# Performance work log

Measured on AMD Instinct MI355X. Metric: run time of the kernel, lower is better.

## Reference

```python
import jax, jax.numpy as jnp
import numpy as np
from functools import reduce

H = W = 4096


def setup_inputs() -> dict:
    key = jax.random.key(0)
    prob = jax.random.uniform(key, (1, 1, H, W), dtype=jnp.float32)
    return {"prob": prob}


def _ccl_8conn(binary):
    """Parallel connected-component labeling, 8-connectivity (skimage connectivity=2).

    Labels are (min linear index in component) + 1; background = 0. This is the
    same partition into components as skimage.measure.label, up to a bijective
    relabeling of the positive label ids.
    Algorithm: iterate [3x3 min-propagation + 2x pointer jumping] until fixpoint
    (label-equivalence / union-find style, O(log diameter)-ish sweeps).
    """
    h, w = binary.shape
    BIG = np.int32(h * w + 2)  # sentinel larger than any valid label
    idx = jnp.arange(h * w, dtype=jnp.int32).reshape(h, w) + 1
    lab0 = jnp.where(binary, idx, 0)

    def sweep(lab):
        # min over 3x3 foreground neighborhood (includes self)
        l = jnp.where(binary, lab, BIG)
        p = jnp.pad(l, 1, constant_values=int(BIG))
        neigh = [p[di:di + h, dj:dj + w] for di in range(3) for dj in range(3)]
        m = reduce(jnp.minimum, neigh)
        m = jnp.where(binary, m, 0)
        # pointer jumping: hop to the label of the pixel we currently point at
        flat = m.reshape(-1)
        for _ in range(2):
            flat = jnp.where(flat > 0, flat[jnp.maximum(flat - 1, 0)], 0)
        return flat.reshape(h, w)

    def cond(c):
        return c[1]

    def body(c):
        lab, _ = c
        new = sweep(lab)
        return new, jnp.any(new != lab)

    lab, _ = jax.lax.while_loop(cond, body, (lab0, jnp.array(True)))
    return lab


def reference(prob):
    binary = jnp.squeeze(prob) > 0.5  # (prob > 0.5).float().squeeze()
    return _ccl_8conn(binary)
```

## Files before the change

kernel.cpp:

```cpp
#include <hip/hip_runtime.h>
#include <limits.h>


constexpr int HH = 4096;
constexpr int WW = 4096;
constexpr int NPIX = HH * WW;
constexpr int TILE = 128;
constexpr int BDIM = TILE / 2;
constexpr int NBLK = BDIM * BDIM;
constexpr int NBOUND = HH / TILE - 1;
constexpr int NSEG = WW / 2;
constexpr int LINKS_PER_FAM = NBOUND * NSEG * 3;

__device__ __forceinline__ int find_root_g(int* P, int x) {
    while (true) {
        int p = P[x];
        if (p == x) return x;
        int gp = P[p];
        if (gp == p) return p;
        atomicMin(&P[x], gp);
        x = gp;
    }
}

__device__ __forceinline__ void unite_g(int* P, int a, int b) {
    while (true) {
        a = find_root_g(P, a);
        b = find_root_g(P, b);
        if (a == b) return;
        if (a > b) { int t = a; a = b; b = t; }
        int old = atomicMin(&P[b], a);
        if (old == b) return;
        b = old;
    }
}

__device__ __forceinline__ int lkey2b(int k) {
    return ((k >> 8) << 6) | ((k & 127) >> 1);
}

__device__ __forceinline__ int find_l(int* par, int bk) {
    while (true) {
        int xb = lkey2b(bk);
        int p = par[xb];
        if (p == bk) return bk;
        int pb = lkey2b(p);
        int gp = par[pb];
        if (gp == p) return p;
        atomicMin(&par[xb], gp);
        bk = gp;
    }
}

__device__ __forceinline__ void unite_l(int* par, int ka, int kb) {
    while (true) {
        ka = find_l(par, ka);
        kb = find_l(par, kb);
        if (ka == kb) return;
        if (ka > kb) { int t = ka; ka = kb; kb = t; }
        int old = atomicMin(&par[lkey2b(kb)], ka);
        if (old == kb) return;
        kb = old;
    }
}

__device__ __forceinline__ int bkey(int b, int m) {
    int base = ((b >> 6) << 8) + ((b & 63) << 1);
    int off = (m & 1) ? 0 : (m & 2) ? 1 : (m & 4) ? 128 : 129;
    return base + off;
}

__global__ __launch_bounds__(512) void ccl_local_bke(const float* __restrict__ prob,
                                                     int* __restrict__ P) {
    __shared__ int bmask[NBLK];
    __shared__ int par[NBLK];
    const int tile_c = blockIdx.x * TILE;
    const int tile_r = blockIdx.y * TILE;
    const int tid = threadIdx.x;

    int nib[8];
    #pragma unroll
    for (int k = 0; k < 8; ++k) {
        int b = tid + 512 * k;
        int i = b >> 6, j = b & 63;
        const float* rp = prob + (size_t)(tile_r + 2 * i) * WW + tile_c + 2 * j;
        float2 t = *reinterpret_cast<const float2*>(rp);
        float2 bo = *reinterpret_cast<const float2*>(rp + WW);
        int m = (t.x > 0.5f ? 1 : 0) | (t.y > 0.5f ? 2 : 0) |
                (bo.x > 0.5f ? 4 : 0) | (bo.y > 0.5f ? 8 : 0);
        nib[k] = m;
        bmask[b] = m;
        par[b] = m ? bkey(b, m) : -1;
    }
    __syncthreads();

    #pragma unroll
    for (int k = 0; k < 8; ++k) {
        int m = nib[k];
        if (!m) continue;
        int b = tid + 512 * k;
        int i = b >> 6, j = b & 63;
        int mk = bkey(b, m);
        if (j > 0) {
            int wm = bmask[b - 1];
            if ((m & 0x5) && (wm & 0xA)) unite_l(par, mk, bkey(b - 1, wm));
        }
        if (i > 0) {
            int nm = bmask[b - BDIM];
            if ((m & 0x3) && (nm & 0xC)) unite_l(par, mk, bkey(b - BDIM, nm));
            if (j > 0) {
                int nwm = bmask[b - BDIM - 1];
                if ((m & 0x1) && (nwm & 0x8)) unite_l(par, mk, bkey(b - BDIM - 1, nwm));
            }
            if (j < BDIM - 1) {
                int nem = bmask[b - BDIM + 1];
                if ((m & 0x2) && (nem & 0x4)) unite_l(par, mk, bkey(b - BDIM + 1, nem));
            }
        }
    }
    __syncthreads();

    #pragma unroll
    for (int k = 0; k < 8; ++k) {
        int b = tid + 512 * k;
        int i = b >> 6, j = b & 63;
        int gr = tile_r + 2 * i, gc = tile_c + 2 * j;
        int m = nib[k];
        int2 top = make_int2(-1, -1), bot = make_int2(-1, -1);
        if (m) {
            int x = bkey(b, m);
            while (true) {
                int p = par[lkey2b(x)];
                if (p == x) break;
                x = p;
            }
            int g = (tile_r + (x >> 7)) * WW + tile_c + (x & 127);
            top.x = (m & 1) ? g : -1;
            top.y = (m & 2) ? g : -1;
            bot.x = (m & 4) ? g : -1;
            bot.y = (m & 8) ? g : -1;
        }
        *reinterpret_cast<int2*>(P + (size_t)gr * WW + gc) = top;
        *reinterpret_cast<int2*>(P + (size_t)(gr + 1) * WW + gc) = bot;
    }
}

__global__ void ccl_border(int* __restrict__ P) {
    int idx = blockIdx.x * 256 + threadIdx.x;
    if (idx >= LINKS_PER_FAM) return;
    int link = idx / (NBOUND * NSEG);
    int rem  = idx - link * (NBOUND * NSEG);
    int bidx = rem >> 11;
    int t    = rem & (NSEG - 1);
    if (blockIdx.y == 0) {
        int r = (bidx + 1) * TILE;
        int c0 = 2 * t;
        if (link == 0) {
            int2 d = *reinterpret_cast<const int2*>(P + (size_t)r * WW + c0);
            int2 u = *reinterpret_cast<const int2*>(P + (size_t)(r - 1) * WW + c0);
            bool d0 = d.x >= 0, d1 = d.y >= 0;
            bool u0 = u.x >= 0, u1 = u.y >= 0;
            if ((d0 | d1) && (u0 | u1)) {
                int pd = d0 ? r * WW + c0 : r * WW + c0 + 1;
                int pu = u0 ? (r - 1) * WW + c0 : (r - 1) * WW + c0 + 1;
                unite_g(P, pd, pu);
            }
        } else if (link == 1) {
            if (c0 > 0 && P[(size_t)r * WW + c0] >= 0 &&
                P[(size_t)(r - 1) * WW + c0 - 1] >= 0)
                unite_g(P, r * WW + c0, (r - 1) * WW + c0 - 1);
        } else {
            if (c0 + 2 < WW && P[(size_t)r * WW + c0 + 1] >= 0 &&
                P[(size_t)(r - 1) * WW + c0 + 2] >= 0)
                unite_g(P, r * WW + c0 + 1, (r - 1) * WW + c0 + 2);
        }
    } else {
        int c = (bidx + 1) * TILE;
        int r0 = 2 * t;
        if (link == 0) {
            bool e0 = P[(size_t)r0 * WW + c] >= 0;
            bool e1 = P[(size_t)(r0 + 1) * WW + c] >= 0;
            bool w0 = P[(size_t)r0 * WW + c - 1] >= 0;
            bool w1 = P[(size_t)(r0 + 1) * WW + c - 1] >= 0;
            if ((e0 | e1) && (w0 | w1)) {
                int pe = e0 ? r0 * WW + c : (r0 + 1) * WW + c;
                int pw = w0 ? r0 * WW + c - 1 : (r0 + 1) * WW + c - 1;
                unite_g(P, pe, pw);
            }
        } else if (link == 1) {
            if (r0 > 0 && P[(size_t)r0 * WW + c] >= 0 &&
                P[(size_t)(r0 - 1) * WW + c - 1] >= 0)
                unite_g(P, r0 * WW + c, (r0 - 1) * WW + c - 1);
        } else {
            if (r0 + 2 < HH && P[(size_t)(r0 + 1) * WW + c] >= 0 &&
                P[(size_t)(r0 + 2) * WW + c - 1] >= 0)
                unite_g(P, (r0 + 1) * WW + c, (r0 + 2) * WW + c - 1);
        }
    }
}

__device__ __forceinline__ int resolve_memo(const int* __restrict__ P, int x,
                                            int& ci, int& co) {
    if (x < 0) return 0;
    if (x == ci) return co;
    int r = x;
    while (true) { int p = P[r]; if (p == r) break; r = p; }
    ci = x; co = r + 1;
    return co;
}

__global__ void ccl_final4(const int* __restrict__ P, int* __restrict__ out) {
    int i = (blockIdx.x * blockDim.x + threadIdx.x) * 4;
    int4 v = *reinterpret_cast<const int4*>(P + i);
    int ci = -2, co = 0;
    int4 o;
    o.x = resolve_memo(P, v.x, ci, co);
    o.y = resolve_memo(P, v.y, ci, co);
    o.z = resolve_memo(P, v.z, ci, co);
    o.w = resolve_memo(P, v.w, ci, co);
    *reinterpret_cast<int4*>(out + i) = o;
}

__global__ void ccl_compress(int* __restrict__ P) {
    int i = blockIdx.x * blockDim.x + threadIdx.x;
    int x = P[i];
    if (x < 0) return;
    while (true) { int p = P[x]; if (p == x) break; x = p; }
    P[i] = x;
}

__global__ void ccl_convert(int* __restrict__ P) {
    int i = (blockIdx.x * blockDim.x + threadIdx.x) * 4;
    int4 v = *reinterpret_cast<const int4*>(P + i);
    v.x = (v.x < 0) ? 0 : v.x + 1;
    v.y = (v.y < 0) ? 0 : v.y + 1;
    v.z = (v.z < 0) ? 0 : v.z + 1;
    v.w = (v.w < 0) ? 0 : v.w + 1;
    *reinterpret_cast<int4*>(P + i) = v;
}

extern "C" void kernel_launch(void* const* d_in, const int* in_sizes, int n_in,
                              void* d_out, int out_size, void* d_ws, size_t ws_size,
                              hipStream_t stream) {
    const float* prob = (const float*)d_in[0];
    const bool have_ws = ws_size >= (size_t)NPIX * sizeof(int);
    int* P = have_ws ? (int*)d_ws : (int*)d_out;

    ccl_local_bke<<<dim3(WW / TILE, HH / TILE), dim3(512), 0, stream>>>(prob, P);

    ccl_border<<<dim3((LINKS_PER_FAM + 255) / 256, 2), dim3(256), 0, stream>>>(P);

    if (have_ws) {
        ccl_final4<<<dim3(NPIX / 4 / 256), dim3(256), 0, stream>>>(P, (int*)d_out);
    } else {
        ccl_compress<<<dim3(NPIX / 256), dim3(256), 0, stream>>>(P);
        ccl_convert<<<dim3(NPIX / 4 / 256), dim3(256), 0, stream>>>(P);
    }
}
```

Measured before the change: 287.4 us.

## Merge border link families per thread and prune redundant unions

The border-merge kernel now handles 4 consecutive boundary pixels per thread instead of one 2-pixel segment per link family. Each thread loads the neighbour labels once with vector loads and reads the stored root labels directly. It skips unions that are already implied by 8-connectivity of adjacent foreground pixels, except at tile-corner positions. This cuts thread count, redundant loads and atomic union traffic, at the cost of more per-thread branching and some uncoalesced strided loads on the vertical boundaries.

Measured after the change: 241.1 us. 1.19x faster.

```diff
diff --git a/kernel.cpp b/kernel.cpp
--- a/kernel.cpp
+++ b/kernel.cpp
@@ -9,8 +9,9 @@
 constexpr int BDIM = TILE / 2;
 constexpr int NBLK = BDIM * BDIM;
 constexpr int NBOUND = HH / TILE - 1;
-constexpr int NSEG = WW / 2;
-constexpr int LINKS_PER_FAM = NBOUND * NSEG * 3;
+constexpr int SEGW = 4;
+constexpr int NSEG4 = WW / SEGW;
+constexpr int THREADS_PER_FAM = NBOUND * NSEG4;
 
 __device__ __forceinline__ int find_root_g(int* P, int x) {
     while (true) {
@@ -147,54 +148,60 @@
 
 __global__ void ccl_border(int* __restrict__ P) {
     int idx = blockIdx.x * 256 + threadIdx.x;
-    if (idx >= LINKS_PER_FAM) return;
-    int link = idx / (NBOUND * NSEG);
-    int rem  = idx - link * (NBOUND * NSEG);
-    int bidx = rem >> 11;
-    int t    = rem & (NSEG - 1);
+    if (idx >= THREADS_PER_FAM) return;
+    int bidx = idx >> 10;
+    int t    = idx & (NSEG4 - 1);
+    int dpar[6], upar[6];
     if (blockIdx.y == 0) {
         int r = (bidx + 1) * TILE;
-        int c0 = 2 * t;
-        if (link == 0) {
-            int2 d = *reinterpret_cast<const int2*>(P + (size_t)r * WW + c0);
-            int2 u = *reinterpret_cast<const int2*>(P + (size_t)(r - 1) * WW + c0);
-            bool d0 = d.x >= 0, d1 = d.y >= 0;
-            bool u0 = u.x >= 0, u1 = u.y >= 0;
-            if ((d0 | d1) && (u0 | u1)) {
-                int pd = d0 ? r * WW + c0 : r * WW + c0 + 1;
-                int pu = u0 ? (r - 1) * WW + c0 : (r - 1) * WW + c0 + 1;
-                unite_g(P, pd, pu);
-            }
-        } else if (link == 1) {
-            if (c0 > 0 && P[(size_t)r * WW + c0] >= 0 &&
-                P[(size_t)(r - 1) * WW + c0 - 1] >= 0)
-                unite_g(P, r * WW + c0, (r - 1) * WW + c0 - 1);
-        } else {
-            if (c0 + 2 < WW && P[(size_t)r * WW + c0 + 1] >= 0 &&
-                P[(size_t)(r - 1) * WW + c0 + 2] >= 0)
-                unite_g(P, r * WW + c0 + 1, (r - 1) * WW + c0 + 2);
+        int c0 = SEGW * t;
+        const int* pd = P + (size_t)r * WW;
+        const int* pu = pd - WW;
+        int4 dv = *reinterpret_cast<const int4*>(pd + c0);
+        int4 uv = *reinterpret_cast<const int4*>(pu + c0);
+        dpar[0] = (c0 > 0) ? pd[c0 - 1] : -1;
+        upar[0] = (c0 > 0) ? pu[c0 - 1] : -1;
+        dpar[1] = dv.x; dpar[2] = dv.y; dpar[3] = dv.z; dpar[4] = dv.w;
+        upar[1] = uv.x; upar[2] = uv.y; upar[3] = uv.z; upar[4] = uv.w;
+        dpar[5] = (c0 + SEGW < WW) ? pd[c0 + SEGW] : -1;
+        upar[5] = (c0 + SEGW < WW) ? pu[c0 + SEGW] : -1;
+        #pragma unroll
+        for (int k = 1; k <= SEGW; ++k) {
+            if (dpar[k] < 0) continue;
+            int c = c0 + k - 1;
+            int j = c & (TILE - 1);
+            bool U  = upar[k] >= 0;
+            bool Dm = dpar[k - 1] >= 0, Um = upar[k - 1] >= 0;
+            bool Dp = dpar[k + 1] >= 0, Up = upar[k + 1] >= 0;
+            if (U  && (j == 0        || !(Dm && Um))) unite_g(P, dpar[k], upar[k]);
+            if (Um && (j == 0        || (!U && !Dm))) unite_g(P, dpar[k], upar[k - 1]);
+            if (Up && (j == TILE - 1 || (!U && !Dp))) unite_g(P, dpar[k], upar[k + 1]);
         }
     } else {
         int c = (bidx + 1) * TILE;
-        int r0 = 2 * t;
-        if (link == 0) {
-            bool e0 = P[(size_t)r0 * WW + c] >= 0;
-            bool e1 = P[(size_t)(r0 + 1) * WW + c] >= 0;
-            bool w0 = P[(size_t)r0 * WW + c - 1] >= 0;
-            bool w1 = P[(size_t)(r0 + 1) * WW + c - 1] >= 0;
-            if ((e0 | e1) && (w0 | w1)) {
-                int pe = e0 ? r0 * WW + c : (r0 + 1) * WW + c;
-                int pw = w0 ? r0 * WW + c - 1 : (r0 + 1) * WW + c - 1;
-                unite_g(P, pe, pw);
-            }
-        } else if (link == 1) {
-            if (r0 > 0 && P[(size_t)r0 * WW + c] >= 0 &&
-                P[(size_t)(r0 - 1) * WW + c - 1] >= 0)
-                unite_g(P, r0 * WW + c, (r0 - 1) * WW + c - 1);
-        } else {
-            if (r0 + 2 < HH && P[(size_t)(r0 + 1) * WW + c] >= 0 &&
-                P[(size_t)(r0 + 2) * WW + c - 1] >= 0)
-                unite_g(P, (r0 + 1) * WW + c, (r0 + 2) * WW + c - 1);
+        int r0 = SEGW * t;
+        const int* pe = P + c;
+        const int* pw = P + c - 1;
+        dpar[0] = (r0 > 0) ? pe[(size_t)(r0 - 1) * WW] : -1;
+        upar[0] = (r0 > 0) ? pw[(size_t)(r0 - 1) * WW] : -1;
+        #pragma unroll
+        for (int k = 1; k <= SEGW; ++k) {
+            dpar[k] = pe[(size_t)(r0 + k - 1) * WW];
+            upar[k] = pw[(size_t)(r0 + k - 1) * WW];
+        }
+        dpar[5] = (r0 + SEGW < HH) ? pe[(size_t)(r0 + SEGW) * WW] : -1;
+        upar[5] = (r0 + SEGW < HH) ? pw[(size_t)(r0 + SEGW) * WW] : -1;
+        #pragma unroll
+        for (int k = 1; k <= SEGW; ++k) {
+            if (dpar[k] < 0) continue;
+            int r = r0 + k - 1;
+            int i = r & (TILE - 1);
+            bool W  = upar[k] >= 0;
+            bool Em = dpar[k - 1] >= 0, Wm = upar[k - 1] >= 0;
+            bool Ep = dpar[k + 1] >= 0, Wp = upar[k + 1] >= 0;
+            if (W  && (i == 0        || !(Em && Wm))) unite_g(P, dpar[k], upar[k]);
+            if (Wm && (i == 0        || (!W && !Em))) unite_g(P, dpar[k], upar[k - 1]);
+            if (Wp && (i == TILE - 1 || (!W && !Ep))) unite_g(P, dpar[k], upar[k + 1]);
         }
     }
 }
@@ -248,7 +255,7 @@
 
     ccl_local_bke<<<dim3(WW / TILE, HH / TILE), dim3(512), 0, stream>>>(prob, P);
 
-    ccl_border<<<dim3((LINKS_PER_FAM + 255) / 256, 2), dim3(256), 0, stream>>>(P);
+    ccl_border<<<dim3((THREADS_PER_FAM + 255) / 256, 2), dim3(256), 0, stream>>>(P);
 
     if (have_ws) {
         ccl_final4<<<dim3(NPIX / 4 / 256), dim3(256), 0, stream>>>(P, (int*)d_out);
```

## Store labels per 2x2 block with packed nibble masks for border and final passes

Applied to the files above, without the earlier changes.

The global union-find array is shrunk to one entry per 2x2 block, indexed by a key-to-block mapping, and each block's foreground nibble is packed eight to a 32-bit word. The border merge now loads the bitmasks, builds 32-bit edge masks and only unites at run starts, so each boundary segment needs far fewer thread slots and memory reads. The final pass resolves eight pixels per thread from the block-level parent array and the nibble bits. This cuts intermediate memory traffic roughly fourfold, at the cost of bit-manipulation complexity. A pixel-level fallback path is kept for when workspace is too small.

New measurement: 296.0 us. +3.0%, slower.

```diff
diff --git a/kernel.cpp b/kernel.cpp
--- a/kernel.cpp
+++ b/kernel.cpp
@@ -8,28 +8,34 @@
 constexpr int TILE = 128;
 constexpr int BDIM = TILE / 2;
 constexpr int NBLK = BDIM * BDIM;
+constexpr int BW = WW / 2;
+constexpr int WPR = BW / 8;
 constexpr int NBOUND = HH / TILE - 1;
-constexpr int NSEG = WW / 2;
-constexpr int LINKS_PER_FAM = NBOUND * NSEG * 3;
-
-__device__ __forceinline__ int find_root_g(int* P, int x) {
-    while (true) {
-        int p = P[x];
-        if (p == x) return x;
-        int gp = P[p];
+constexpr int BTHREADS = NBOUND * (WW / 32);
+
+__device__ __forceinline__ int blkof(int key) {
+    return ((key >> 13) << 11) | ((key & 4095) >> 1);
+}
+
+__device__ __forceinline__ int find_B(int* P, int key) {
+    while (true) {
+        int xb = blkof(key);
+        int p = P[xb];
+        if (p == key) return key;
+        int gp = P[blkof(p)];
         if (gp == p) return p;
-        atomicMin(&P[x], gp);
-        x = gp;
-    }
-}
-
-__device__ __forceinline__ void unite_g(int* P, int a, int b) {
-    while (true) {
-        a = find_root_g(P, a);
-        b = find_root_g(P, b);
+        atomicMin(&P[xb], gp);
+        key = gp;
+    }
+}
+
+__device__ __forceinline__ void unite_B(int* P, int a, int b) {
+    while (true) {
+        a = find_B(P, a);
+        b = find_B(P, b);
         if (a == b) return;
         if (a > b) { int t = a; a = b; b = t; }
-        int old = atomicMin(&P[b], a);
+        int old = atomicMin(&P[blkof(b)], a);
         if (old == b) return;
         b = old;
     }
@@ -71,11 +77,14 @@
 }
 
 __global__ __launch_bounds__(512) void ccl_local_bke(const float* __restrict__ prob,
-                                                     int* __restrict__ P) {
+                                                     int* __restrict__ Pb,
+                                                     unsigned int* __restrict__ bnib) {
     __shared__ int bmask[NBLK];
     __shared__ int par[NBLK];
     const int tile_c = blockIdx.x * TILE;
     const int tile_r = blockIdx.y * TILE;
+    const int tile_bj = blockIdx.x * BDIM;
+    const int tile_bi = blockIdx.y * BDIM;
     const int tid = threadIdx.x;
 
     int nib[8];
@@ -124,9 +133,8 @@
     for (int k = 0; k < 8; ++k) {
         int b = tid + 512 * k;
         int i = b >> 6, j = b & 63;
-        int gr = tile_r + 2 * i, gc = tile_c + 2 * j;
         int m = nib[k];
-        int2 top = make_int2(-1, -1), bot = make_int2(-1, -1);
+        int val = -1;
         if (m) {
             int x = bkey(b, m);
             while (true) {
@@ -134,93 +142,178 @@
                 if (p == x) break;
                 x = p;
             }
-            int g = (tile_r + (x >> 7)) * WW + tile_c + (x & 127);
-            top.x = (m & 1) ? g : -1;
-            top.y = (m & 2) ? g : -1;
-            bot.x = (m & 4) ? g : -1;
-            bot.y = (m & 8) ? g : -1;
-        }
-        *reinterpret_cast<int2*>(P + (size_t)gr * WW + gc) = top;
-        *reinterpret_cast<int2*>(P + (size_t)(gr + 1) * WW + gc) = bot;
-    }
-}
-
-__global__ void ccl_border(int* __restrict__ P) {
+            val = (tile_r + (x >> 7)) * WW + tile_c + (x & 127);
+        }
+        Pb[(size_t)(tile_bi + i) * BW + tile_bj + j] = val;
+    }
+
+    {
+        unsigned int word = 0;
+        #pragma unroll
+        for (int q = 0; q < 8; ++q)
+            word |= (unsigned int)bmask[8 * tid + q] << (4 * q);
+        int i = (8 * tid) >> 6;
+        int wj = ((8 * tid) & 63) >> 3;
+        bnib[(size_t)(tile_bi + i) * WPR + (tile_bj >> 3) + wj] = word;
+    }
+}
+
+__device__ __forceinline__ unsigned int ext01(unsigned int w) {
+    unsigned int b = w & 0x33333333u;
+    b = (b | (b >> 2)) & 0x0F0F0F0Fu;
+    b = (b | (b >> 4)) & 0x00FF00FFu;
+    b = (b | (b >> 8)) & 0x0000FFFFu;
+    return b;
+}
+__device__ __forceinline__ unsigned int ext23(unsigned int w) { return ext01(w >> 2); }
+
+__global__ void ccl_border(int* __restrict__ Pb,
+                           const unsigned int* __restrict__ bnib) {
     int idx = blockIdx.x * 256 + threadIdx.x;
-    if (idx >= LINKS_PER_FAM) return;
-    int link = idx / (NBOUND * NSEG);
-    int rem  = idx - link * (NBOUND * NSEG);
-    int bidx = rem >> 11;
-    int t    = rem & (NSEG - 1);
+    if (idx >= BTHREADS) return;
+    int bidx = idx >> 7;
+    int w    = idx & 127;
+    unsigned int edge0  = ((w & 3) == 0) ? 1u : 0u;
+    unsigned int edge31 = ((w & 3) == 3) ? 0x80000000u : 0u;
+
     if (blockIdx.y == 0) {
         int r = (bidx + 1) * TILE;
-        int c0 = 2 * t;
-        if (link == 0) {
-            int2 d = *reinterpret_cast<const int2*>(P + (size_t)r * WW + c0);
-            int2 u = *reinterpret_cast<const int2*>(P + (size_t)(r - 1) * WW + c0);
-            bool d0 = d.x >= 0, d1 = d.y >= 0;
-            bool u0 = u.x >= 0, u1 = u.y >= 0;
-            if ((d0 | d1) && (u0 | u1)) {
-                int pd = d0 ? r * WW + c0 : r * WW + c0 + 1;
-                int pu = u0 ? (r - 1) * WW + c0 : (r - 1) * WW + c0 + 1;
-                unite_g(P, pd, pu);
-            }
-        } else if (link == 1) {
-            if (c0 > 0 && P[(size_t)r * WW + c0] >= 0 &&
-                P[(size_t)(r - 1) * WW + c0 - 1] >= 0)
-                unite_g(P, r * WW + c0, (r - 1) * WW + c0 - 1);
-        } else {
-            if (c0 + 2 < WW && P[(size_t)r * WW + c0 + 1] >= 0 &&
-                P[(size_t)(r - 1) * WW + c0 + 2] >= 0)
-                unite_g(P, r * WW + c0 + 1, (r - 1) * WW + c0 + 2);
-        }
+        int bi_d = r >> 1, bi_u = bi_d - 1;
+        int c0 = 32 * w;
+        const unsigned int* rd = bnib + (size_t)bi_d * WPR;
+        const unsigned int* ru = bnib + (size_t)bi_u * WPR;
+        unsigned int D = ext01(rd[2 * w]) | (ext01(rd[2 * w + 1]) << 16);
+        unsigned int U = ext23(ru[2 * w]) | (ext23(ru[2 * w + 1]) << 16);
+        unsigned int dm1 = 0, um1 = 0, dp1 = 0, up1 = 0;
+        if (c0 > 0) {
+            dm1 = (rd[2 * w - 1] >> 29) & 1;
+            um1 = (ru[2 * w - 1] >> 31) & 1;
+        }
+        if (c0 + 32 < WW) {
+            dp1 = rd[2 * w + 2] & 1;
+            up1 = (ru[2 * w + 2] >> 2) & 1;
+        }
+        unsigned int Dprev = (D << 1) | dm1, Uprev = (U << 1) | um1;
+        unsigned int Dnext = (D >> 1) | (dp1 << 31), Unext = (U >> 1) | (up1 << 31);
+        unsigned int Nm  = D & U     & (~(Dprev & Uprev) | edge0);
+        unsigned int NWm = D & Uprev & ((~U & ~Dprev)    | edge0);
+        unsigned int NEm = D & Unext & ((~U & ~Dnext)    | edge31);
+        int baseD = r * WW + c0, baseU = baseD - WW;
+        while (Nm)  { int k = __ffs(Nm)  - 1; Nm  &= Nm  - 1; unite_B(Pb, baseD + k, baseU + k); }
+        while (NWm) { int k = __ffs(NWm) - 1; NWm &= NWm - 1; unite_B(Pb, baseD + k, baseU + k - 1); }
+        while (NEm) { int k = __ffs(NEm) - 1; NEm &= NEm - 1; unite_B(Pb, baseD + k, baseU + k + 1); }
     } else {
         int c = (bidx + 1) * TILE;
-        int r0 = 2 * t;
-        if (link == 0) {
-            bool e0 = P[(size_t)r0 * WW + c] >= 0;
-            bool e1 = P[(size_t)(r0 + 1) * WW + c] >= 0;
-            bool w0 = P[(size_t)r0 * WW + c - 1] >= 0;
-            bool w1 = P[(size_t)(r0 + 1) * WW + c - 1] >= 0;
-            if ((e0 | e1) && (w0 | w1)) {
-                int pe = e0 ? r0 * WW + c : (r0 + 1) * WW + c;
-                int pw = w0 ? r0 * WW + c - 1 : (r0 + 1) * WW + c - 1;
-                unite_g(P, pe, pw);
-            }
-        } else if (link == 1) {
-            if (r0 > 0 && P[(size_t)r0 * WW + c] >= 0 &&
-                P[(size_t)(r0 - 1) * WW + c - 1] >= 0)
-                unite_g(P, r0 * WW + c, (r0 - 1) * WW + c - 1);
-        } else {
-            if (r0 + 2 < HH && P[(size_t)(r0 + 1) * WW + c] >= 0 &&
-                P[(size_t)(r0 + 2) * WW + c - 1] >= 0)
-                unite_g(P, (r0 + 1) * WW + c, (r0 + 2) * WW + c - 1);
-        }
-    }
-}
-
-__device__ __forceinline__ int resolve_memo(const int* __restrict__ P, int x,
-                                            int& ci, int& co) {
-    if (x < 0) return 0;
+        int bj_e = c >> 1, bj_w = bj_e - 1;
+        int r0 = 32 * w;
+        int bi0 = r0 >> 1;
+        int we_idx = bj_e >> 3;
+        int ww_idx = bj_w >> 3;
+        unsigned int E = 0, W = 0;
+        #pragma unroll
+        for (int q = 0; q < 16; ++q) {
+            unsigned int ne = bnib[(size_t)(bi0 + q) * WPR + we_idx] & 0xF;
+            unsigned int nw = (bnib[(size_t)(bi0 + q) * WPR + ww_idx] >> 28) & 0xF;
+            E |= (((ne >> 0) & 1) | (((ne >> 2) & 1) << 1)) << (2 * q);
+            W |= (((nw >> 1) & 1) | (((nw >> 3) & 1) << 1)) << (2 * q);
+        }
+        unsigned int em1 = 0, wm1 = 0, ep1 = 0, wp1 = 0;
+        if (r0 > 0) {
+            em1 = (bnib[(size_t)(bi0 - 1) * WPR + we_idx] >> 2) & 1;
+            wm1 = (bnib[(size_t)(bi0 - 1) * WPR + ww_idx] >> 31) & 1;
+        }
+        if (r0 + 32 < HH) {
+            ep1 = bnib[(size_t)(bi0 + 16) * WPR + we_idx] & 1;
+            wp1 = (bnib[(size_t)(bi0 + 16) * WPR + ww_idx] >> 29) & 1;
+        }
+        unsigned int Eprev = (E << 1) | em1, Wprev = (W << 1) | wm1;
+        unsigned int Enext = (E >> 1) | (ep1 << 31), Wnext = (W >> 1) | (wp1 << 31);
+        unsigned int Wl  = E & W     & (~(Eprev & Wprev) | edge0);
+        unsigned int NWl = E & Wprev & ((~W & ~Eprev)    | edge0);
+        unsigned int SWl = E & Wnext & ((~W & ~Enext)    | edge31);
+        while (Wl)  { int k = __ffs(Wl)  - 1; Wl  &= Wl  - 1; unite_B(Pb, (r0 + k) * WW + c, (r0 + k) * WW + c - 1); }
+        while (NWl) { int k = __ffs(NWl) - 1; NWl &= NWl - 1; unite_B(Pb, (r0 + k) * WW + c, (r0 + k - 1) * WW + c - 1); }
+        while (SWl) { int k = __ffs(SWl) - 1; SWl &= SWl - 1; unite_B(Pb, (r0 + k) * WW + c, (r0 + k + 1) * WW + c - 1); }
+    }
+}
+
+__device__ __forceinline__ int resolveB(const int* __restrict__ P, int x,
+                                        int& ci, int& co) {
     if (x == ci) return co;
     int r = x;
-    while (true) { int p = P[r]; if (p == r) break; r = p; }
+    while (true) { int p = P[blkof(r)]; if (p == r) break; r = p; }
     ci = x; co = r + 1;
     return co;
 }
 
-__global__ void ccl_final4(const int* __restrict__ P, int* __restrict__ out) {
+__global__ void ccl_final8(const int* __restrict__ Pb,
+                           const unsigned int* __restrict__ bnib,
+                           int* __restrict__ out) {
+    int t = blockIdx.x * 256 + threadIdx.x;
+    int base = t * 8;
+    int r = base >> 12, c0 = base & 4095;
+    unsigned int nibs = bnib[(size_t)(r >> 1) * WPR + (c0 >> 4)] >> (4 * ((c0 >> 1) & 7));
+    int4 pv = *reinterpret_cast<const int4*>(Pb + (size_t)(r >> 1) * BW + (c0 >> 1));
+    const int* pvp = reinterpret_cast<const int*>(&pv);
+    int rowsh = (r & 1) << 1;
+    int lab[8];
+    int ci = INT_MIN, co = 0;
+    #pragma unroll
+    for (int q = 0; q < 8; ++q) {
+        int nb = (nibs >> (4 * (q >> 1))) & 0xF;
+        int bit = (nb >> (rowsh | (q & 1))) & 1;
+        lab[q] = bit ? resolveB(Pb, pvp[q >> 1], ci, co) : 0;
+    }
+    *reinterpret_cast<int4*>(out + base)     = make_int4(lab[0], lab[1], lab[2], lab[3]);
+    *reinterpret_cast<int4*>(out + base + 4) = make_int4(lab[4], lab[5], lab[6], lab[7]);
+}
+
+__device__ __forceinline__ int find_root_g(int* P, int x) {
+    while (true) {
+        int p = P[x];
+        if (p == x) return x;
+        int gp = P[p];
+        if (gp == p) return p;
+        atomicMin(&P[x], gp);
+        x = gp;
+    }
+}
+__device__ __forceinline__ void unite_g(int* P, int a, int b) {
+    while (true) {
+        a = find_root_g(P, a);
+        b = find_root_g(P, b);
+        if (a == b) return;
+        if (a > b) { int t = a; a = b; b = t; }
+        int old = atomicMin(&P[b], a);
+        if (old == b) return;
+        b = old;
+    }
+}
+__global__ void ccl_init_px(const float* __restrict__ prob, int* __restrict__ P) {
     int i = (blockIdx.x * blockDim.x + threadIdx.x) * 4;
-    int4 v = *reinterpret_cast<const int4*>(P + i);
-    int ci = -2, co = 0;
+    float4 v = *reinterpret_cast<const float4*>(prob + i);
     int4 o;
-    o.x = resolve_memo(P, v.x, ci, co);
-    o.y = resolve_memo(P, v.y, ci, co);
-    o.z = resolve_memo(P, v.z, ci, co);
-    o.w = resolve_memo(P, v.w, ci, co);
-    *reinterpret_cast<int4*>(out + i) = o;
-}
-
+    o.x = (v.x > 0.5f) ? i : -1;
+    o.y = (v.y > 0.5f) ? i + 1 : -1;
+    o.z = (v.z > 0.5f) ? i + 2 : -1;
+    o.w = (v.w > 0.5f) ? i + 3 : -1;
+    *reinterpret_cast<int4*>(P + i) = o;
+}
+__global__ void ccl_merge_px(int* __restrict__ P) {
+    int c = blockIdx.x * blockDim.x + threadIdx.x;
+    int r = blockIdx.y * blockDim.y + threadIdx.y;
+    int i = r * WW + c;
+    if (P[i] < 0) return;
+    if (c > 0 && P[i - 1] >= 0) unite_g(P, i, i - 1);
+    if (r > 0) {
+        int j = i - WW;
+        if (P[j] >= 0) unite_g(P, i, j);
+        else {
+            if (c > 0      && P[j - 1] >= 0) unite_g(P, i, j - 1);
+            if (c < WW - 1 && P[j + 1] >= 0) unite_g(P, i, j + 1);
+        }
+    }
+}
 __global__ void ccl_compress(int* __restrict__ P) {
     int i = blockIdx.x * blockDim.x + threadIdx.x;
     int x = P[i];
@@ -228,7 +321,6 @@
     while (true) { int p = P[x]; if (p == x) break; x = p; }
     P[i] = x;
 }
-
 __global__ void ccl_convert(int* __restrict__ P) {
     int i = (blockIdx.x * blockDim.x + threadIdx.x) * 4;
     int4 v = *reinterpret_cast<const int4*>(P + i);
@@ -243,16 +335,21 @@
                               void* d_out, int out_size, void* d_ws, size_t ws_size,
                               hipStream_t stream) {
     const float* prob = (const float*)d_in[0];
-    const bool have_ws = ws_size >= (size_t)NPIX * sizeof(int);
-    int* P = have_ws ? (int*)d_ws : (int*)d_out;
-
-    ccl_local_bke<<<dim3(WW / TILE, HH / TILE), dim3(512), 0, stream>>>(prob, P);
-
-    ccl_border<<<dim3((LINKS_PER_FAM + 255) / 256, 2), dim3(256), 0, stream>>>(P);
+    const size_t PB_BYTES = (size_t)(BW * BW) * sizeof(int);
+    const size_t BN_BYTES = (size_t)(BW * WPR) * sizeof(unsigned);
+    const bool have_ws = ws_size >= PB_BYTES + BN_BYTES;
 
     if (have_ws) {
-        ccl_final4<<<dim3(NPIX / 4 / 256), dim3(256), 0, stream>>>(P, (int*)d_out);
+        int* Pb = (int*)d_ws;
+        unsigned int* bnib = (unsigned int*)((char*)d_ws + PB_BYTES);
+
+        ccl_local_bke<<<dim3(WW / TILE, HH / TILE), dim3(512), 0, stream>>>(prob, Pb, bnib);
+        ccl_border<<<dim3((BTHREADS + 255) / 256, 2), dim3(256), 0, stream>>>(Pb, bnib);
+        ccl_final8<<<dim3(NPIX / 8 / 256), dim3(256), 0, stream>>>(Pb, bnib, (int*)d_out);
     } else {
+        int* P = (int*)d_out;
+        ccl_init_px<<<dim3(NPIX / 4 / 256), dim3(256), 0, stream>>>(prob, P);
+        ccl_merge_px<<<dim3(WW / 64, HH / 4), dim3(64, 4), 0, stream>>>(P);
         ccl_compress<<<dim3(NPIX / 256), dim3(256), 0, stream>>>(P);
         ccl_convert<<<dim3(NPIX / 4 / 256), dim3(256), 0, stream>>>(P);
     }
```
